# Kernel optimization log

Hardware: AMD Instinct MI355X
Metric: run time of the kernel (lower is better)

## Reference

```python
import jax, jax.numpy as jnp
import numpy as np

B, OUT, IN = 4096, 1024, 1024
BN_EPS = 1e-5


def setup_inputs() -> dict:
    key = jax.random.key(0)
    kx, k1, k2, k3 = jax.random.split(key, 4)
    # kaiming_uniform_ with a=sqrt(5): bound = sqrt(6 / ((1+a^2) * fan_in)) = 1/sqrt(fan_in)
    bound = 1.0 / np.sqrt(IN)
    x = jax.random.normal(kx, (B, IN), dtype=jnp.float32)
    c1 = jax.random.uniform(k1, (OUT, IN), jnp.float32, -bound, bound)
    c2 = jax.random.uniform(k2, (OUT, IN), jnp.float32, -bound, bound)
    c3 = jax.random.uniform(k3, (OUT, IN), jnp.float32, -bound, bound)
    bias = jnp.zeros((OUT, IN), jnp.float32)
    gamma = jnp.ones((OUT,), jnp.float32)   # BatchNorm1d weight
    beta = jnp.zeros((OUT,), jnp.float32)   # BatchNorm1d bias
    return {"x": x, "c1": c1, "c2": c2, "c3": c3, "bias": bias,
            "gamma": gamma, "beta": beta}


def reference(x, c1, c2, c3, bias, gamma, beta):
    # Fused polynomial 'matmul': out[b,o] = sum_i x*c1 + x^2*c2 + x^3*c3 + bias
    x2 = x * x
    x3 = x2 * x
    y = (jnp.einsum('bi,oi->bo', x, c1)
         + jnp.einsum('bi,oi->bo', x2, c2)
         + jnp.einsum('bi,oi->bo', x3, c3)
         + jnp.sum(bias, axis=1))  # bias reduced over in_features
    # BatchNorm1d (training mode: batch statistics, biased variance)
    mean = jnp.mean(y, axis=0)
    var = jnp.var(y, axis=0)
    return (y - mean) * jax.lax.rsqrt(var + BN_EPS) * gamma + beta
```

## Files before the change

kernel.cpp:

```cpp
#include <hip/hip_runtime.h>
#include <stdint.h>

#define B_ROWS 4096
#define OUTF   1024
#define INF    1024
#define KTOT   3072
#define BN_EPS 1e-5f
#define BM 128
#define BN 128
#define BK 64
#define NSTEP (KTOT / BK)

typedef short  short8  __attribute__((ext_vector_type(8)));
typedef float  floatx4 __attribute__((ext_vector_type(4)));

struct alignas(8) s4 { short x, y, z, w; };

__device__ __forceinline__ short f2bf(float f) {
  union { float f; uint32_t u; } cv; cv.f = f;
  uint32_t u = cv.u;
  uint32_t r = (u + 0x7fffu + ((u >> 16) & 1u)) >> 16;
  return (short)r;
}

__device__ __forceinline__ void load_lds16(const void* g, void* l) {
  __builtin_amdgcn_global_load_lds(
      (const __attribute__((address_space(1))) uint32_t*)(uintptr_t)g,
      (__attribute__((address_space(3))) uint32_t*)(uint32_t)(uintptr_t)l,
      16, 0, 0);
}

__global__ void prep_all(const float4* __restrict__ x4,
                         const float4* __restrict__ c1, const float4* __restrict__ c2,
                         const float4* __restrict__ c3, const float* __restrict__ bias,
                         short* __restrict__ Xb, short* __restrict__ Wb,
                         float* __restrict__ biassum) {
  int b = blockIdx.x;
  if (b < 4096) {
    int idx = b * 256 + threadIdx.x;
    float4 v = x4[idx];
    int row = idx >> 8;
    int c   = (idx & 255) << 2;
    size_t base = (size_t)row * KTOT + c;
    s4 p1 = { f2bf(v.x), f2bf(v.y), f2bf(v.z), f2bf(v.w) };
    float ax = v.x * v.x, ay = v.y * v.y, az = v.z * v.z, aw = v.w * v.w;
    s4 p2 = { f2bf(ax), f2bf(ay), f2bf(az), f2bf(aw) };
    s4 p3 = { f2bf(ax * v.x), f2bf(ay * v.y), f2bf(az * v.z), f2bf(aw * v.w) };
    *(s4*)&Xb[base]        = p1;
    *(s4*)&Xb[base + 1024] = p2;
    *(s4*)&Xb[base + 2048] = p3;
  } else if (b < 5120) {
    int idx = (b - 4096) * 256 + threadIdx.x;
    int row = idx >> 8;
    int c   = (idx & 255) << 2;
    size_t base = (size_t)row * KTOT + c;
    float4 a = c1[idx], bb = c2[idx], d = c3[idx];
    s4 p1 = { f2bf(a.x),  f2bf(a.y),  f2bf(a.z),  f2bf(a.w)  };
    s4 p2 = { f2bf(bb.x), f2bf(bb.y), f2bf(bb.z), f2bf(bb.w) };
    s4 p3 = { f2bf(d.x),  f2bf(d.y),  f2bf(d.z),  f2bf(d.w)  };
    *(s4*)&Wb[base]        = p1;
    *(s4*)&Wb[base + 1024] = p2;
    *(s4*)&Wb[base + 2048] = p3;
  } else {
    int o = (b - 5120) * 4 + (threadIdx.x >> 6);
    int l = threadIdx.x & 63;
    const float4* bp = (const float4*)(bias + (size_t)o * INF);
    float s = 0.f;
    for (int i = l; i < 256; i += 64) { float4 v = bp[i]; s += v.x + v.y + v.z + v.w; }
    #pragma unroll
    for (int off = 32; off; off >>= 1) s += __shfl_down(s, off, 64);
    if (l == 0) biassum[o] = s;
  }
}

__global__ __launch_bounds__(512, 2) void gemm_poly(
    const short* __restrict__ Xb, const short* __restrict__ Wb,
    const float* __restrict__ biassum, float* __restrict__ Y,
    float* __restrict__ psum, float* __restrict__ psq) {
  __shared__ __align__(16) short As[2][BM * BK];
  __shared__ __align__(16) short Bs[2][BN * BK];
  const int tid  = threadIdx.x;
  const int lane = tid & 63;
  const int wave = tid >> 6;
  const int wr = wave >> 2;
  const int wc = wave & 3;
  const int lb  = blockIdx.x;
  const int xcd = lb & 7;
  const int sl  = lb >> 3;
  const int bx  = sl & 7;
  const int by  = xcd * 4 + (sl >> 3);
  const int row0 = by * BM;
  const int col0 = bx * BN;
  const short* Ag = Xb + (size_t)row0 * KTOT;
  const short* Bg = Wb + (size_t)col0 * KTOT;
  const int frag_m = lane & 15;
  const int sel = lane >> 4;
  floatx4 acc[4][2] = {};

  int off01[2];
  #pragma unroll
  for (int i = 0; i < 2; ++i) {
    int c = tid + i * 512;
    int r = c >> 3, p = c & 7;
    int lg = p ^ (r & 7);
    off01[i] = r * KTOT + lg * 8;
  }

  #pragma unroll
  for (int i = 0; i < 2; ++i) {
    load_lds16(Ag + off01[i], &As[0][(tid + i * 512) * 8]);
    load_lds16(Bg + off01[i], &Bs[0][(tid + i * 512) * 8]);
  }

  for (int step = 0; step < NSTEP; ++step) {
    __syncthreads();
    const int cur = step & 1;
    if (step + 1 < NSTEP) {
      const int kt = (step + 1) * BK;
      const int nxt = cur ^ 1;
      #pragma unroll
      for (int i = 0; i < 2; ++i) {
        load_lds16(Ag + off01[i] + kt, &As[nxt][(tid + i * 512) * 8]);
        load_lds16(Bg + off01[i] + kt, &Bs[nxt][(tid + i * 512) * 8]);
      }
    }
    #pragma unroll
    for (int s = 0; s < 2; ++s) {
      short8 af[4], bfr[2];
      #pragma unroll
      for (int i = 0; i < 4; ++i) {
        int r = wr * 64 + i * 16 + frag_m;
        int p = (s * 4 + sel) ^ (r & 7);
        af[i] = *(const short8*)&As[cur][r * BK + p * 8];
      }
      #pragma unroll
      for (int j = 0; j < 2; ++j) {
        int r = wc * 32 + j * 16 + frag_m;
        int p = (s * 4 + sel) ^ (r & 7);
        bfr[j] = *(const short8*)&Bs[cur][r * BK + p * 8];
      }
      #pragma unroll
      for (int i = 0; i < 4; ++i)
        #pragma unroll
        for (int j = 0; j < 2; ++j)
          acc[i][j] = __builtin_amdgcn_mfma_f32_16x16x32_bf16(af[i], bfr[j], acc[i][j], 0, 0, 0);
    }
  }

  float* colred = (float*)&As[0][0];
  const int drow = sel << 2;
  const int dcol = frag_m;
  float sv[2] = {0.f, 0.f}, sq[2] = {0.f, 0.f};
  #pragma unroll
  for (int j = 0; j < 2; ++j) {
    int gc = col0 + wc * 32 + j * 16 + dcol;
    float bsv = biassum[gc];
    #pragma unroll
    for (int i = 0; i < 4; ++i) {
      int gr = row0 + wr * 64 + i * 16 + drow;
      #pragma unroll
      for (int r = 0; r < 4; ++r) {
        float v = acc[i][j][r] + bsv;
        Y[(size_t)(gr + r) * OUTF + gc] = v;
        sv[j] += v; sq[j] += v * v;
      }
    }
  }
  #pragma unroll
  for (int j = 0; j < 2; ++j) {
    sv[j] += __shfl_xor(sv[j], 16, 64); sv[j] += __shfl_xor(sv[j], 32, 64);
    sq[j] += __shfl_xor(sq[j], 16, 64); sq[j] += __shfl_xor(sq[j], 32, 64);
  }
  if (sel == 0) {
    #pragma unroll
    for (int j = 0; j < 2; ++j) {
      int cc = wc * 32 + j * 16 + dcol;
      colred[wr * 256 + cc]       = sv[j];
      colred[wr * 256 + 128 + cc] = sq[j];
    }
  }
  __syncthreads();
  if (tid < BN) {
    float ssum = colred[tid]       + colred[256 + tid];
    float ssq  = colred[128 + tid] + colred[384 + tid];
    psum[(size_t)by * OUTF + col0 + tid] = ssum;
    psq [(size_t)by * OUTF + col0 + tid] = ssq;
  }
}

__global__ void bn_fused(const float* __restrict__ psum, const float* __restrict__ psq,
                         const float* __restrict__ gamma, const float* __restrict__ beta,
                         float* __restrict__ Y) {
  __shared__ float sc[32], sh[32];
  const int c0 = blockIdx.x * 32;
  const int t = threadIdx.x;
  if (t < 32) {
    float s = 0.f, s2 = 0.f;
    #pragma unroll 8
    for (int p = 0; p < 32; ++p) {
      s  += psum[p * OUTF + c0 + t];
      s2 += psq [p * OUTF + c0 + t];
    }
    float mean = s * (1.0f / B_ROWS);
    float var  = s2 * (1.0f / B_ROWS) - mean * mean;
    float scale = gamma[c0 + t] * rsqrtf(var + BN_EPS);
    sc[t] = scale;
    sh[t] = beta[c0 + t] - mean * scale;
  }
  __syncthreads();
  const int f4c = t & 7;
  const int rr  = t >> 3;
  const int row0 = blockIdx.y * 256;
  float4* Y4 = (float4*)Y;
  const int cb = f4c * 4;
  float s0 = sc[cb], s1 = sc[cb+1], s2 = sc[cb+2], s3 = sc[cb+3];
  float h0 = sh[cb], h1 = sh[cb+1], h2 = sh[cb+2], h3 = sh[cb+3];
  #pragma unroll
  for (int it = 0; it < 8; ++it) {
    int row = row0 + it * 32 + rr;
    size_t idx = (size_t)row * 256 + (c0 >> 2) + f4c;
    float4 v = Y4[idx];
    v.x = v.x * s0 + h0; v.y = v.y * s1 + h1;
    v.z = v.z * s2 + h2; v.w = v.w * s3 + h3;
    Y4[idx] = v;
  }
}

extern "C" void kernel_launch(void* const* d_in, const int* in_sizes, int n_in,
                              void* d_out, int out_size, void* d_ws, size_t ws_size,
                              hipStream_t stream) {
  const float* x     = (const float*)d_in[0];
  const float* c1    = (const float*)d_in[1];
  const float* c2    = (const float*)d_in[2];
  const float* c3    = (const float*)d_in[3];
  const float* bias  = (const float*)d_in[4];
  const float* gamma = (const float*)d_in[5];
  const float* beta  = (const float*)d_in[6];
  float* out = (float*)d_out;
  char* ws = (char*)d_ws;

  short* Xb      = (short*)(ws);
  short* Wb      = (short*)(ws + 25165824);
  float* biassum = (float*)(ws + 31457280);
  float* psum    = (float*)(ws + 31461376);
  float* psq     = (float*)(ws + 31592448);

  prep_all<<<5376, 256, 0, stream>>>((const float4*)x, (const float4*)c1,
                                     (const float4*)c2, (const float4*)c3,
                                     bias, Xb, Wb, biassum);

  gemm_poly<<<256, 512, 0, stream>>>(Xb, Wb, biassum, out, psum, psq);

  dim3 bgrid(OUTF / 32, B_ROWS / 256);
  bn_fused<<<bgrid, 256, 0, stream>>>(psum, psq, gamma, beta, out);
}
```

Baseline: 130.7 us.

## Fuse prep, GEMM and batchnorm into one cooperative kernel with grid syncs

Merges the bf16 conversion pass, the polynomial GEMM and the batchnorm apply into a single cooperative kernel. Two grid-wide syncs separate the phases: one after the inputs are converted, one after the per-tile column statistics are written. After the second sync each block keeps its accumulators in registers and writes the normalized output directly. This removes the separate launches and the write-then-reread of the unnormalized Y. The bias reduction is dropped because a per-column constant cancels under batch-statistic normalization. The cost is two grid barriers and a dependency on all blocks being co-resident, plus the prep work now being spread over only 256 blocks.

```diff
diff --git a/kernel.cpp b/kernel.cpp
--- a/kernel.cpp
+++ b/kernel.cpp
@@ -1,5 +1,8 @@
 #include <hip/hip_runtime.h>
+#include <hip/hip_cooperative_groups.h>
 #include <stdint.h>
+
+namespace cg = cooperative_groups;
 
 #define B_ROWS 4096
 #define OUTF   1024
@@ -30,61 +33,59 @@
       16, 0, 0);
 }
 
-__global__ void prep_all(const float4* __restrict__ x4,
-                         const float4* __restrict__ c1, const float4* __restrict__ c2,
-                         const float4* __restrict__ c3, const float* __restrict__ bias,
-                         short* __restrict__ Xb, short* __restrict__ Wb,
-                         float* __restrict__ biassum) {
-  int b = blockIdx.x;
-  if (b < 4096) {
-    int idx = b * 256 + threadIdx.x;
-    float4 v = x4[idx];
-    int row = idx >> 8;
-    int c   = (idx & 255) << 2;
-    size_t base = (size_t)row * KTOT + c;
-    s4 p1 = { f2bf(v.x), f2bf(v.y), f2bf(v.z), f2bf(v.w) };
-    float ax = v.x * v.x, ay = v.y * v.y, az = v.z * v.z, aw = v.w * v.w;
-    s4 p2 = { f2bf(ax), f2bf(ay), f2bf(az), f2bf(aw) };
-    s4 p3 = { f2bf(ax * v.x), f2bf(ay * v.y), f2bf(az * v.z), f2bf(aw * v.w) };
-    *(s4*)&Xb[base]        = p1;
-    *(s4*)&Xb[base + 1024] = p2;
-    *(s4*)&Xb[base + 2048] = p3;
-  } else if (b < 5120) {
-    int idx = (b - 4096) * 256 + threadIdx.x;
-    int row = idx >> 8;
-    int c   = (idx & 255) << 2;
-    size_t base = (size_t)row * KTOT + c;
-    float4 a = c1[idx], bb = c2[idx], d = c3[idx];
-    s4 p1 = { f2bf(a.x),  f2bf(a.y),  f2bf(a.z),  f2bf(a.w)  };
-    s4 p2 = { f2bf(bb.x), f2bf(bb.y), f2bf(bb.z), f2bf(bb.w) };
-    s4 p3 = { f2bf(d.x),  f2bf(d.y),  f2bf(d.z),  f2bf(d.w)  };
-    *(s4*)&Wb[base]        = p1;
-    *(s4*)&Wb[base + 1024] = p2;
-    *(s4*)&Wb[base + 2048] = p3;
-  } else {
-    int o = (b - 5120) * 4 + (threadIdx.x >> 6);
-    int l = threadIdx.x & 63;
-    const float4* bp = (const float4*)(bias + (size_t)o * INF);
-    float s = 0.f;
-    for (int i = l; i < 256; i += 64) { float4 v = bp[i]; s += v.x + v.y + v.z + v.w; }
-    #pragma unroll
-    for (int off = 32; off; off >>= 1) s += __shfl_down(s, off, 64);
-    if (l == 0) biassum[o] = s;
-  }
-}
-
-__global__ __launch_bounds__(512, 2) void gemm_poly(
-    const short* __restrict__ Xb, const short* __restrict__ Wb,
-    const float* __restrict__ biassum, float* __restrict__ Y,
-    float* __restrict__ psum, float* __restrict__ psq) {
+__global__ __launch_bounds__(512, 2) void fused_all(
+    const float4* __restrict__ x4,
+    const float4* __restrict__ c1, const float4* __restrict__ c2,
+    const float4* __restrict__ c3,
+    const float* __restrict__ gamma, const float* __restrict__ beta,
+    short* __restrict__ Xb, short* __restrict__ Wb,
+    float* __restrict__ psum, float* __restrict__ psq,
+    float* __restrict__ Y) {
   __shared__ __align__(16) short As[2][BM * BK];
   __shared__ __align__(16) short Bs[2][BN * BK];
-  const int tid  = threadIdx.x;
+  const int tid = threadIdx.x;
+  const int lb  = blockIdx.x;
+  cg::grid_group grid = cg::this_grid();
+
+  {
+    int gt = lb * 512 + tid;
+    #pragma unroll
+    for (int it = 0; it < 8; ++it) {
+      int idx = it * 131072 + gt;
+      float4 v = x4[idx];
+      int row = idx >> 8;
+      int c   = (idx & 255) << 2;
+      size_t base = (size_t)row * KTOT + c;
+      s4 p1 = { f2bf(v.x), f2bf(v.y), f2bf(v.z), f2bf(v.w) };
+      float ax = v.x * v.x, ay = v.y * v.y, az = v.z * v.z, aw = v.w * v.w;
+      s4 p2 = { f2bf(ax), f2bf(ay), f2bf(az), f2bf(aw) };
+      s4 p3 = { f2bf(ax * v.x), f2bf(ay * v.y), f2bf(az * v.z), f2bf(aw * v.w) };
+      *(s4*)&Xb[base]        = p1;
+      *(s4*)&Xb[base + 1024] = p2;
+      *(s4*)&Xb[base + 2048] = p3;
+    }
+    #pragma unroll
+    for (int it = 0; it < 2; ++it) {
+      int idx = it * 131072 + gt;
+      int row = idx >> 8;
+      int c   = (idx & 255) << 2;
+      size_t base = (size_t)row * KTOT + c;
+      float4 a = c1[idx], bb = c2[idx], d = c3[idx];
+      s4 p1 = { f2bf(a.x),  f2bf(a.y),  f2bf(a.z),  f2bf(a.w)  };
+      s4 p2 = { f2bf(bb.x), f2bf(bb.y), f2bf(bb.z), f2bf(bb.w) };
+      s4 p3 = { f2bf(d.x),  f2bf(d.y),  f2bf(d.z),  f2bf(d.w)  };
+      *(s4*)&Wb[base]        = p1;
+      *(s4*)&Wb[base + 1024] = p2;
+      *(s4*)&Wb[base + 2048] = p3;
+    }
+  }
+  __threadfence();
+  grid.sync();
+
   const int lane = tid & 63;
   const int wave = tid >> 6;
   const int wr = wave >> 2;
   const int wc = wave & 3;
-  const int lb  = blockIdx.x;
   const int xcd = lb & 7;
   const int sl  = lb >> 3;
   const int bx  = sl & 7;
@@ -148,24 +149,16 @@
   }
 
   float* colred = (float*)&As[0][0];
-  const int drow = sel << 2;
-  const int dcol = frag_m;
   float sv[2] = {0.f, 0.f}, sq[2] = {0.f, 0.f};
   #pragma unroll
-  for (int j = 0; j < 2; ++j) {
-    int gc = col0 + wc * 32 + j * 16 + dcol;
-    float bsv = biassum[gc];
-    #pragma unroll
-    for (int i = 0; i < 4; ++i) {
-      int gr = row0 + wr * 64 + i * 16 + drow;
+  for (int j = 0; j < 2; ++j)
+    #pragma unroll
+    for (int i = 0; i < 4; ++i)
       #pragma unroll
       for (int r = 0; r < 4; ++r) {
-        float v = acc[i][j][r] + bsv;
-        Y[(size_t)(gr + r) * OUTF + gc] = v;
+        float v = acc[i][j][r];
         sv[j] += v; sq[j] += v * v;
       }
-    }
-  }
   #pragma unroll
   for (int j = 0; j < 2; ++j) {
     sv[j] += __shfl_xor(sv[j], 16, 64); sv[j] += __shfl_xor(sv[j], 32, 64);
@@ -174,55 +167,48 @@
   if (sel == 0) {
     #pragma unroll
     for (int j = 0; j < 2; ++j) {
-      int cc = wc * 32 + j * 16 + dcol;
+      int cc = wc * 32 + j * 16 + frag_m;
       colred[wr * 256 + cc]       = sv[j];
       colred[wr * 256 + 128 + cc] = sq[j];
     }
   }
   __syncthreads();
   if (tid < BN) {
-    float ssum = colred[tid]       + colred[256 + tid];
-    float ssq  = colred[128 + tid] + colred[384 + tid];
-    psum[(size_t)by * OUTF + col0 + tid] = ssum;
-    psq [(size_t)by * OUTF + col0 + tid] = ssq;
-  }
-}
-
-__global__ void bn_fused(const float* __restrict__ psum, const float* __restrict__ psq,
-                         const float* __restrict__ gamma, const float* __restrict__ beta,
-                         float* __restrict__ Y) {
-  __shared__ float sc[32], sh[32];
-  const int c0 = blockIdx.x * 32;
-  const int t = threadIdx.x;
-  if (t < 32) {
+    psum[(size_t)by * OUTF + col0 + tid] = colred[tid]       + colred[256 + tid];
+    psq [(size_t)by * OUTF + col0 + tid] = colred[128 + tid] + colred[384 + tid];
+  }
+  __threadfence();
+  grid.sync();
+
+  float* cscale = (float*)&Bs[0][0];
+  float* cshift = cscale + 128;
+  if (tid < BN) {
     float s = 0.f, s2 = 0.f;
     #pragma unroll 8
     for (int p = 0; p < 32; ++p) {
-      s  += psum[p * OUTF + c0 + t];
-      s2 += psq [p * OUTF + c0 + t];
+      s  += psum[(size_t)p * OUTF + col0 + tid];
+      s2 += psq [(size_t)p * OUTF + col0 + tid];
     }
     float mean = s * (1.0f / B_ROWS);
     float var  = s2 * (1.0f / B_ROWS) - mean * mean;
-    float scale = gamma[c0 + t] * rsqrtf(var + BN_EPS);
-    sc[t] = scale;
-    sh[t] = beta[c0 + t] - mean * scale;
+    float sc = gamma[col0 + tid] * rsqrtf(var + BN_EPS);
+    cscale[tid] = sc;
+    cshift[tid] = beta[col0 + tid] - mean * sc;
   }
   __syncthreads();
-  const int f4c = t & 7;
-  const int rr  = t >> 3;
-  const int row0 = blockIdx.y * 256;
-  float4* Y4 = (float4*)Y;
-  const int cb = f4c * 4;
-  float s0 = sc[cb], s1 = sc[cb+1], s2 = sc[cb+2], s3 = sc[cb+3];
-  float h0 = sh[cb], h1 = sh[cb+1], h2 = sh[cb+2], h3 = sh[cb+3];
-  #pragma unroll
-  for (int it = 0; it < 8; ++it) {
-    int row = row0 + it * 32 + rr;
-    size_t idx = (size_t)row * 256 + (c0 >> 2) + f4c;
-    float4 v = Y4[idx];
-    v.x = v.x * s0 + h0; v.y = v.y * s1 + h1;
-    v.z = v.z * s2 + h2; v.w = v.w * s3 + h3;
-    Y4[idx] = v;
+  const int drow = sel << 2;
+  #pragma unroll
+  for (int j = 0; j < 2; ++j) {
+    int cc = wc * 32 + j * 16 + frag_m;
+    float sc = cscale[cc], sh = cshift[cc];
+    int gc = col0 + cc;
+    #pragma unroll
+    for (int i = 0; i < 4; ++i) {
+      int gr = row0 + wr * 64 + i * 16 + drow;
+      #pragma unroll
+      for (int r = 0; r < 4; ++r)
+        Y[(size_t)(gr + r) * OUTF + gc] = acc[i][j][r] * sc + sh;
+    }
   }
 }
 
@@ -233,24 +219,20 @@
   const float* c1    = (const float*)d_in[1];
   const float* c2    = (const float*)d_in[2];
   const float* c3    = (const float*)d_in[3];
-  const float* bias  = (const float*)d_in[4];
   const float* gamma = (const float*)d_in[5];
   const float* beta  = (const float*)d_in[6];
   float* out = (float*)d_out;
   char* ws = (char*)d_ws;
 
-  short* Xb      = (short*)(ws);
-  short* Wb      = (short*)(ws + 25165824);
-  float* biassum = (float*)(ws + 31457280);
-  float* psum    = (float*)(ws + 31461376);
-  float* psq     = (float*)(ws + 31592448);
-
-  prep_all<<<5376, 256, 0, stream>>>((const float4*)x, (const float4*)c1,
-                                     (const float4*)c2, (const float4*)c3,
-                                     bias, Xb, Wb, biassum);
-
-  gemm_poly<<<256, 512, 0, stream>>>(Xb, Wb, biassum, out, psum, psq);
-
-  dim3 bgrid(OUTF / 32, B_ROWS / 256);
-  bn_fused<<<bgrid, 256, 0, stream>>>(psum, psq, gamma, beta, out);
-}
+  short* Xb   = (short*)(ws);
+  short* Wb   = (short*)(ws + 25165824);
+  float* psum = (float*)(ws + 31457280);
+  float* psq  = (float*)(ws + 31588352);
+
+  void* args[] = { (void*)&x, (void*)&c1, (void*)&c2, (void*)&c3,
+                   (void*)&gamma, (void*)&beta,
+                   (void*)&Xb, (void*)&Wb, (void*)&psum, (void*)&psq,
+                   (void*)&out };
+  hipLaunchCooperativeKernel((void*)fused_all, dim3(256), dim3(512),
+                             args, 0, stream);
+}
```

Result: slower. 298.5 us (+128.4%).

## Triple-buffer GEMM LDS pipeline and drop bias reduction cancelled by BatchNorm

Applied to the files above, without the earlier changes.

The GEMM main loop moves from double to triple LDS buffering, so global-to-LDS loads are prefetched two K-steps ahead. It syncs with an explicit vmcnt wait plus a raw barrier instead of __syncthreads, aiming to hide global load latency better. The bias row-sum is removed entirely, since a per-feature constant is subtracted out by the batch-mean in training-mode BatchNorm. That saves a 4 MB read and some prep blocks. The cost is 50% more LDS per block, which may pressure the 2-blocks-per-CU occupancy target, and the hand-coded waitcnt immediates are fragile.

```diff
diff --git a/kernel.cpp b/kernel.cpp
--- a/kernel.cpp
+++ b/kernel.cpp
@@ -16,6 +16,9 @@
 
 struct alignas(8) s4 { short x, y, z, w; };
 
+#define WAIT_VM4 0x0F74
+#define WAIT_VM0 0x0F70
+
 __device__ __forceinline__ short f2bf(float f) {
   union { float f; uint32_t u; } cv; cv.f = f;
   uint32_t u = cv.u;
@@ -32,9 +35,8 @@
 
 __global__ void prep_all(const float4* __restrict__ x4,
                          const float4* __restrict__ c1, const float4* __restrict__ c2,
-                         const float4* __restrict__ c3, const float* __restrict__ bias,
-                         short* __restrict__ Xb, short* __restrict__ Wb,
-                         float* __restrict__ biassum) {
+                         const float4* __restrict__ c3,
+                         short* __restrict__ Xb, short* __restrict__ Wb) {
   int b = blockIdx.x;
   if (b < 4096) {
     int idx = b * 256 + threadIdx.x;
@@ -49,7 +51,7 @@
     *(s4*)&Xb[base]        = p1;
     *(s4*)&Xb[base + 1024] = p2;
     *(s4*)&Xb[base + 2048] = p3;
-  } else if (b < 5120) {
+  } else {
     int idx = (b - 4096) * 256 + threadIdx.x;
     int row = idx >> 8;
     int c   = (idx & 255) << 2;
@@ -61,24 +63,14 @@
     *(s4*)&Wb[base]        = p1;
     *(s4*)&Wb[base + 1024] = p2;
     *(s4*)&Wb[base + 2048] = p3;
-  } else {
-    int o = (b - 5120) * 4 + (threadIdx.x >> 6);
-    int l = threadIdx.x & 63;
-    const float4* bp = (const float4*)(bias + (size_t)o * INF);
-    float s = 0.f;
-    for (int i = l; i < 256; i += 64) { float4 v = bp[i]; s += v.x + v.y + v.z + v.w; }
-    #pragma unroll
-    for (int off = 32; off; off >>= 1) s += __shfl_down(s, off, 64);
-    if (l == 0) biassum[o] = s;
   }
 }
 
 __global__ __launch_bounds__(512, 2) void gemm_poly(
     const short* __restrict__ Xb, const short* __restrict__ Wb,
-    const float* __restrict__ biassum, float* __restrict__ Y,
-    float* __restrict__ psum, float* __restrict__ psq) {
-  __shared__ __align__(16) short As[2][BM * BK];
-  __shared__ __align__(16) short Bs[2][BN * BK];
+    float* __restrict__ Y, float* __restrict__ psum, float* __restrict__ psq) {
+  __shared__ __align__(16) short As[3][BM * BK];
+  __shared__ __align__(16) short Bs[3][BN * BK];
   const int tid  = threadIdx.x;
   const int lane = tid & 63;
   const int wave = tid >> 6;
@@ -111,80 +103,97 @@
     load_lds16(Ag + off01[i], &As[0][(tid + i * 512) * 8]);
     load_lds16(Bg + off01[i], &Bs[0][(tid + i * 512) * 8]);
   }
-
-  for (int step = 0; step < NSTEP; ++step) {
-    __syncthreads();
-    const int cur = step & 1;
-    if (step + 1 < NSTEP) {
-      const int kt = (step + 1) * BK;
-      const int nxt = cur ^ 1;
+  #pragma unroll
+  for (int i = 0; i < 2; ++i) {
+    load_lds16(Ag + off01[i] + BK, &As[1][(tid + i * 512) * 8]);
+    load_lds16(Bg + off01[i] + BK, &Bs[1][(tid + i * 512) * 8]);
+  }
+
+#define GSTEP(CUR, PRE, KT_PRE, DO_PRE, WAITIMM)                              \
+  {                                                                           \
+    __builtin_amdgcn_s_waitcnt(WAITIMM);                                      \
+    __builtin_amdgcn_s_barrier();                                             \
+    if (DO_PRE) {                                                             \
+      _Pragma("unroll")                                                       \
+      for (int i = 0; i < 2; ++i) {                                           \
+        load_lds16(Ag + off01[i] + (KT_PRE), &As[PRE][(tid + i * 512) * 8]);  \
+        load_lds16(Bg + off01[i] + (KT_PRE), &Bs[PRE][(tid + i * 512) * 8]);  \
+      }                                                                       \
+    }                                                                         \
+    _Pragma("unroll")                                                         \
+    for (int s = 0; s < 2; ++s) {                                             \
+      short8 af[4], bfr[2];                                                   \
+      _Pragma("unroll")                                                       \
+      for (int i = 0; i < 4; ++i) {                                           \
+        int r = wr * 64 + i * 16 + frag_m;                                    \
+        int p = (s * 4 + sel) ^ (r & 7);                                      \
+        af[i] = *(const short8*)&As[CUR][r * BK + p * 8];                     \
+      }                                                                       \
+      _Pragma("unroll")                                                       \
+      for (int j = 0; j < 2; ++j) {                                           \
+        int r = wc * 32 + j * 16 + frag_m;                                    \
+        int p = (s * 4 + sel) ^ (r & 7);                                      \
+        bfr[j] = *(const short8*)&Bs[CUR][r * BK + p * 8];                    \
+      }                                                                       \
+      _Pragma("unroll")                                                       \
+      for (int i = 0; i < 4; ++i)                                             \
+        _Pragma("unroll")                                                     \
+        for (int j = 0; j < 2; ++j)                                           \
+          acc[i][j] = __builtin_amdgcn_mfma_f32_16x16x32_bf16(                \
+              af[i], bfr[j], acc[i][j], 0, 0, 0);                             \
+    }                                                                         \
+  }
+
+  for (int t3 = 0; t3 < 45; t3 += 3) {
+    GSTEP(0, 2, (t3 + 2) * BK, 1, WAIT_VM4);
+    GSTEP(1, 0, (t3 + 3) * BK, 1, WAIT_VM4);
+    GSTEP(2, 1, (t3 + 4) * BK, 1, WAIT_VM4);
+  }
+  GSTEP(0, 2, 47 * BK, 1, WAIT_VM4);
+  GSTEP(1, 0, 0, 0, WAIT_VM4);
+  GSTEP(2, 0, 0, 0, WAIT_VM0);
+#undef GSTEP
+
+  float* colred = (float*)&As[0][0];
+  float sv[2] = {0.f, 0.f}, sq[2] = {0.f, 0.f};
+  #pragma unroll
+  for (int j = 0; j < 2; ++j)
+    #pragma unroll
+    for (int i = 0; i < 4; ++i)
       #pragma unroll
-      for (int i = 0; i < 2; ++i) {
-        load_lds16(Ag + off01[i] + kt, &As[nxt][(tid + i * 512) * 8]);
-        load_lds16(Bg + off01[i] + kt, &Bs[nxt][(tid + i * 512) * 8]);
+      for (int r = 0; r < 4; ++r) {
+        float v = acc[i][j][r];
+        sv[j] += v; sq[j] += v * v;
       }
+  #pragma unroll
+  for (int j = 0; j < 2; ++j) {
+    sv[j] += __shfl_xor(sv[j], 16, 64); sv[j] += __shfl_xor(sv[j], 32, 64);
+    sq[j] += __shfl_xor(sq[j], 16, 64); sq[j] += __shfl_xor(sq[j], 32, 64);
+  }
+  if (sel == 0) {
+    #pragma unroll
+    for (int j = 0; j < 2; ++j) {
+      int cc = wc * 32 + j * 16 + frag_m;
+      colred[wr * 256 + cc]       = sv[j];
+      colred[wr * 256 + 128 + cc] = sq[j];
     }
-    #pragma unroll
-    for (int s = 0; s < 2; ++s) {
-      short8 af[4], bfr[2];
-      #pragma unroll
-      for (int i = 0; i < 4; ++i) {
-        int r = wr * 64 + i * 16 + frag_m;
-        int p = (s * 4 + sel) ^ (r & 7);
-        af[i] = *(const short8*)&As[cur][r * BK + p * 8];
-      }
-      #pragma unroll
-      for (int j = 0; j < 2; ++j) {
-        int r = wc * 32 + j * 16 + frag_m;
-        int p = (s * 4 + sel) ^ (r & 7);
-        bfr[j] = *(const short8*)&Bs[cur][r * BK + p * 8];
-      }
-      #pragma unroll
-      for (int i = 0; i < 4; ++i)
-        #pragma unroll
-        for (int j = 0; j < 2; ++j)
-          acc[i][j] = __builtin_amdgcn_mfma_f32_16x16x32_bf16(af[i], bfr[j], acc[i][j], 0, 0, 0);
-    }
-  }
-
-  float* colred = (float*)&As[0][0];
+  }
   const int drow = sel << 2;
-  const int dcol = frag_m;
-  float sv[2] = {0.f, 0.f}, sq[2] = {0.f, 0.f};
   #pragma unroll
   for (int j = 0; j < 2; ++j) {
-    int gc = col0 + wc * 32 + j * 16 + dcol;
-    float bsv = biassum[gc];
+    int gc = col0 + wc * 32 + j * 16 + frag_m;
     #pragma unroll
     for (int i = 0; i < 4; ++i) {
       int gr = row0 + wr * 64 + i * 16 + drow;
       #pragma unroll
-      for (int r = 0; r < 4; ++r) {
-        float v = acc[i][j][r] + bsv;
-        Y[(size_t)(gr + r) * OUTF + gc] = v;
-        sv[j] += v; sq[j] += v * v;
-      }
-    }
-  }
-  #pragma unroll
-  for (int j = 0; j < 2; ++j) {
-    sv[j] += __shfl_xor(sv[j], 16, 64); sv[j] += __shfl_xor(sv[j], 32, 64);
-    sq[j] += __shfl_xor(sq[j], 16, 64); sq[j] += __shfl_xor(sq[j], 32, 64);
-  }
-  if (sel == 0) {
-    #pragma unroll
-    for (int j = 0; j < 2; ++j) {
-      int cc = wc * 32 + j * 16 + dcol;
-      colred[wr * 256 + cc]       = sv[j];
-      colred[wr * 256 + 128 + cc] = sq[j];
+      for (int r = 0; r < 4; ++r)
+        Y[(size_t)(gr + r) * OUTF + gc] = acc[i][j][r];
     }
   }
   __syncthreads();
   if (tid < BN) {
-    float ssum = colred[tid]       + colred[256 + tid];
-    float ssq  = colred[128 + tid] + colred[384 + tid];
-    psum[(size_t)by * OUTF + col0 + tid] = ssum;
-    psq [(size_t)by * OUTF + col0 + tid] = ssq;
+    psum[(size_t)by * OUTF + col0 + tid] = colred[tid]       + colred[256 + tid];
+    psq [(size_t)by * OUTF + col0 + tid] = colred[128 + tid] + colred[384 + tid];
   }
 }
 
@@ -233,23 +242,21 @@
   const float* c1    = (const float*)d_in[1];
   const float* c2    = (const float*)d_in[2];
   const float* c3    = (const float*)d_in[3];
-  const float* bias  = (const float*)d_in[4];
   const float* gamma = (const float*)d_in[5];
   const float* beta  = (const float*)d_in[6];
   float* out = (float*)d_out;
   char* ws = (char*)d_ws;
 
-  short* Xb      = (short*)(ws);
-  short* Wb      = (short*)(ws + 25165824);
-  float* biassum = (float*)(ws + 31457280);
-  float* psum    = (float*)(ws + 31461376);
-  float* psq     = (float*)(ws + 31592448);
-
-  prep_all<<<5376, 256, 0, stream>>>((const float4*)x, (const float4*)c1,
+  short* Xb   = (short*)(ws);
+  short* Wb   = (short*)(ws + 25165824);
+  float* psum = (float*)(ws + 31457280);
+  float* psq  = (float*)(ws + 31588352);
+
+  prep_all<<<5120, 256, 0, stream>>>((const float4*)x, (const float4*)c1,
                                      (const float4*)c2, (const float4*)c3,
-                                     bias, Xb, Wb, biassum);
-
-  gemm_poly<<<256, 512, 0, stream>>>(Xb, Wb, biassum, out, psum, psq);
+                                     Xb, Wb);
+
+  gemm_poly<<<256, 512, 0, stream>>>(Xb, Wb, out, psum, psq);
 
   dim3 bgrid(OUTF / 32, B_ROWS / 256);
   bn_fused<<<bgrid, 256, 0, stream>>>(psum, psq, gamma, beta, out);
```

Result: faster. 124.3 us (-4.9%).

## Drop bias reduction cancelled by BatchNorm and double GEMM K-tile depth

Applied to the files above, without the earlier changes.

The per-feature bias sum is a per-column constant, and training-mode BatchNorm subtracts the column mean, so the constant cancels exactly. The bias read, the reduction branch in prep and the biassum buffer are therefore removed, which saves reading the 4 MB bias array. The GEMM K tile also grows from 64 to 128, with a wider XOR swizzle, which halves the number of barrier-separated main-loop steps. The cost is 128 KB of LDS per block, which rules out two resident blocks per CU. The epilogue is also reordered so the column-statistic LDS writes come before the Y stores.

```diff
diff --git a/kernel.cpp b/kernel.cpp
--- a/kernel.cpp
+++ b/kernel.cpp
@@ -8,7 +8,7 @@
 #define BN_EPS 1e-5f
 #define BM 128
 #define BN 128
-#define BK 64
+#define BK 128
 #define NSTEP (KTOT / BK)
 
 typedef short  short8  __attribute__((ext_vector_type(8)));
@@ -32,9 +32,8 @@
 
 __global__ void prep_all(const float4* __restrict__ x4,
                          const float4* __restrict__ c1, const float4* __restrict__ c2,
-                         const float4* __restrict__ c3, const float* __restrict__ bias,
-                         short* __restrict__ Xb, short* __restrict__ Wb,
-                         float* __restrict__ biassum) {
+                         const float4* __restrict__ c3,
+                         short* __restrict__ Xb, short* __restrict__ Wb) {
   int b = blockIdx.x;
   if (b < 4096) {
     int idx = b * 256 + threadIdx.x;
@@ -49,7 +48,7 @@
     *(s4*)&Xb[base]        = p1;
     *(s4*)&Xb[base + 1024] = p2;
     *(s4*)&Xb[base + 2048] = p3;
-  } else if (b < 5120) {
+  } else {
     int idx = (b - 4096) * 256 + threadIdx.x;
     int row = idx >> 8;
     int c   = (idx & 255) << 2;
@@ -61,22 +60,12 @@
     *(s4*)&Wb[base]        = p1;
     *(s4*)&Wb[base + 1024] = p2;
     *(s4*)&Wb[base + 2048] = p3;
-  } else {
-    int o = (b - 5120) * 4 + (threadIdx.x >> 6);
-    int l = threadIdx.x & 63;
-    const float4* bp = (const float4*)(bias + (size_t)o * INF);
-    float s = 0.f;
-    for (int i = l; i < 256; i += 64) { float4 v = bp[i]; s += v.x + v.y + v.z + v.w; }
-    #pragma unroll
-    for (int off = 32; off; off >>= 1) s += __shfl_down(s, off, 64);
-    if (l == 0) biassum[o] = s;
   }
 }
 
 __global__ __launch_bounds__(512, 2) void gemm_poly(
     const short* __restrict__ Xb, const short* __restrict__ Wb,
-    const float* __restrict__ biassum, float* __restrict__ Y,
-    float* __restrict__ psum, float* __restrict__ psq) {
+    float* __restrict__ Y, float* __restrict__ psum, float* __restrict__ psq) {
   __shared__ __align__(16) short As[2][BM * BK];
   __shared__ __align__(16) short Bs[2][BN * BK];
   const int tid  = threadIdx.x;
@@ -97,19 +86,19 @@
   const int sel = lane >> 4;
   floatx4 acc[4][2] = {};
 
-  int off01[2];
-  #pragma unroll
-  for (int i = 0; i < 2; ++i) {
+  int off4[4];
+  #pragma unroll
+  for (int i = 0; i < 4; ++i) {
     int c = tid + i * 512;
-    int r = c >> 3, p = c & 7;
-    int lg = p ^ (r & 7);
-    off01[i] = r * KTOT + lg * 8;
-  }
-
-  #pragma unroll
-  for (int i = 0; i < 2; ++i) {
-    load_lds16(Ag + off01[i], &As[0][(tid + i * 512) * 8]);
-    load_lds16(Bg + off01[i], &Bs[0][(tid + i * 512) * 8]);
+    int r = c >> 4, p = c & 15;
+    int l = p ^ (r & 15);
+    off4[i] = r * KTOT + l * 8;
+  }
+
+  #pragma unroll
+  for (int i = 0; i < 4; ++i) {
+    load_lds16(Ag + off4[i], &As[0][(tid + i * 512) * 8]);
+    load_lds16(Bg + off4[i], &Bs[0][(tid + i * 512) * 8]);
   }
 
   for (int step = 0; step < NSTEP; ++step) {
@@ -119,24 +108,24 @@
       const int kt = (step + 1) * BK;
       const int nxt = cur ^ 1;
       #pragma unroll
-      for (int i = 0; i < 2; ++i) {
-        load_lds16(Ag + off01[i] + kt, &As[nxt][(tid + i * 512) * 8]);
-        load_lds16(Bg + off01[i] + kt, &Bs[nxt][(tid + i * 512) * 8]);
-      }
-    }
-    #pragma unroll
-    for (int s = 0; s < 2; ++s) {
+      for (int i = 0; i < 4; ++i) {
+        load_lds16(Ag + off4[i] + kt, &As[nxt][(tid + i * 512) * 8]);
+        load_lds16(Bg + off4[i] + kt, &Bs[nxt][(tid + i * 512) * 8]);
+      }
+    }
+    #pragma unroll
+    for (int s = 0; s < 4; ++s) {
       short8 af[4], bfr[2];
       #pragma unroll
       for (int i = 0; i < 4; ++i) {
         int r = wr * 64 + i * 16 + frag_m;
-        int p = (s * 4 + sel) ^ (r & 7);
+        int p = (s * 4 + sel) ^ (r & 15);
         af[i] = *(const short8*)&As[cur][r * BK + p * 8];
       }
       #pragma unroll
       for (int j = 0; j < 2; ++j) {
         int r = wc * 32 + j * 16 + frag_m;
-        int p = (s * 4 + sel) ^ (r & 7);
+        int p = (s * 4 + sel) ^ (r & 15);
         bfr[j] = *(const short8*)&Bs[cur][r * BK + p * 8];
       }
       #pragma unroll
@@ -148,43 +137,46 @@
   }
 
   float* colred = (float*)&As[0][0];
-  const int drow = sel << 2;
-  const int dcol = frag_m;
   float sv[2] = {0.f, 0.f}, sq[2] = {0.f, 0.f};
   #pragma unroll
-  for (int j = 0; j < 2; ++j) {
-    int gc = col0 + wc * 32 + j * 16 + dcol;
-    float bsv = biassum[gc];
-    #pragma unroll
-    for (int i = 0; i < 4; ++i) {
-      int gr = row0 + wr * 64 + i * 16 + drow;
+  for (int j = 0; j < 2; ++j)
+    #pragma unroll
+    for (int i = 0; i < 4; ++i)
       #pragma unroll
       for (int r = 0; r < 4; ++r) {
-        float v = acc[i][j][r] + bsv;
-        Y[(size_t)(gr + r) * OUTF + gc] = v;
+        float v = acc[i][j][r];
         sv[j] += v; sq[j] += v * v;
       }
-    }
-  }
   #pragma unroll
   for (int j = 0; j < 2; ++j) {
     sv[j] += __shfl_xor(sv[j], 16, 64); sv[j] += __shfl_xor(sv[j], 32, 64);
     sq[j] += __shfl_xor(sq[j], 16, 64); sq[j] += __shfl_xor(sq[j], 32, 64);
   }
+  __syncthreads();
   if (sel == 0) {
     #pragma unroll
     for (int j = 0; j < 2; ++j) {
-      int cc = wc * 32 + j * 16 + dcol;
+      int cc = wc * 32 + j * 16 + frag_m;
       colred[wr * 256 + cc]       = sv[j];
       colred[wr * 256 + 128 + cc] = sq[j];
     }
   }
+  const int drow = sel << 2;
+  #pragma unroll
+  for (int j = 0; j < 2; ++j) {
+    int gc = col0 + wc * 32 + j * 16 + frag_m;
+    #pragma unroll
+    for (int i = 0; i < 4; ++i) {
+      int gr = row0 + wr * 64 + i * 16 + drow;
+      #pragma unroll
+      for (int r = 0; r < 4; ++r)
+        Y[(size_t)(gr + r) * OUTF + gc] = acc[i][j][r];
+    }
+  }
   __syncthreads();
   if (tid < BN) {
-    float ssum = colred[tid]       + colred[256 + tid];
-    float ssq  = colred[128 + tid] + colred[384 + tid];
-    psum[(size_t)by * OUTF + col0 + tid] = ssum;
-    psq [(size_t)by * OUTF + col0 + tid] = ssq;
+    psum[(size_t)by * OUTF + col0 + tid] = colred[tid]       + colred[256 + tid];
+    psq [(size_t)by * OUTF + col0 + tid] = colred[128 + tid] + colred[384 + tid];
   }
 }
 
@@ -233,23 +225,21 @@
   const float* c1    = (const float*)d_in[1];
   const float* c2    = (const float*)d_in[2];
   const float* c3    = (const float*)d_in[3];
-  const float* bias  = (const float*)d_in[4];
   const float* gamma = (const float*)d_in[5];
   const float* beta  = (const float*)d_in[6];
   float* out = (float*)d_out;
   char* ws = (char*)d_ws;
 
-  short* Xb      = (short*)(ws);
-  short* Wb      = (short*)(ws + 25165824);
-  float* biassum = (float*)(ws + 31457280);
-  float* psum    = (float*)(ws + 31461376);
-  float* psq     = (float*)(ws + 31592448);
-
-  prep_all<<<5376, 256, 0, stream>>>((const float4*)x, (const float4*)c1,
+  short* Xb   = (short*)(ws);
+  short* Wb   = (short*)(ws + 25165824);
+  float* psum = (float*)(ws + 31457280);
+  float* psq  = (float*)(ws + 31588352);
+
+  prep_all<<<5120, 256, 0, stream>>>((const float4*)x, (const float4*)c1,
                                      (const float4*)c2, (const float4*)c3,
-                                     bias, Xb, Wb, biassum);
-
-  gemm_poly<<<256, 512, 0, stream>>>(Xb, Wb, biassum, out, psum, psq);
+                                     Xb, Wb);
+
+  gemm_poly<<<256, 512, 0, stream>>>(Xb, Wb, out, psum, psq);
 
   dim3 bgrid(OUTF / 32, B_ROWS / 256);
   bn_fused<<<bgrid, 256, 0, stream>>>(psum, psq, gamma, beta, out);
```

Result: faster. 127.3 us (-2.6%).
